# Kernel optimization log

Hardware: AMD Instinct MI355X
Metric: run time of the kernel (lower is better)

The kernel has to match this reference:

```python
import jax, jax.numpy as jnp
import numpy as np
from jax import lax

T, B, I, N, C, L = 512, 256, 64, 512, 10, 3
TAU = 2.0  # train_tau=False -> constant, non-trainable


def setup_inputs() -> dict:
    key = jax.random.key(0)
    ks = jax.random.split(key, 12)
    f32 = jnp.float32
    data = jax.random.normal(ks[0], (T, B, I), f32)
    h0 = 0.1 * jax.random.uniform(ks[1], (L, B, N), f32)  # matches 0.1*torch.rand init
    # Linear params; weights stored as [in, out] so y = x @ W + b
    Win = jax.random.normal(ks[2], (I, N), f32) / np.float32(np.sqrt(I))
    b_in = 0.01 * jax.random.normal(ks[3], (N,), f32)
    Whh = jax.random.normal(ks[4], (L, N, N), f32) / np.float32(np.sqrt(N))
    b_hh = 0.01 * jax.random.normal(ks[5], (L, N), f32)
    Whi = jax.random.normal(ks[6], (L - 1, N, N), f32) / np.float32(np.sqrt(N))
    b_hi = 0.01 * jax.random.normal(ks[7], (L - 1, N), f32)
    Wfc = jax.random.normal(ks[8], (N, C), f32) / np.float32(np.sqrt(N))
    b_fc = 0.01 * jax.random.normal(ks[9], (C,), f32)
    return {"data": data, "h0": h0, "Win": Win, "b_in": b_in,
            "Whh": Whh, "b_hh": b_hh, "Whi": Whi, "b_hi": b_hi,
            "Wfc": Wfc, "b_fc": b_fc}


def reference(data, h0, Win, b_in, Whh, b_hh, Whi, b_hi, Wfc, b_fc):
    alpha = 1.0 - 1.0 / TAU
    # forward() zeroes the recurrent diagonal every call
    Whh = Whh * (1.0 - jnp.eye(N, dtype=Whh.dtype))
    x = data @ Win + b_in  # [T, B, N] input projection (single input layer, mean over 1)

    def step(hs, inp):
        h0_, h1_, h2_ = hs
        # layer 0: leaky integration + LeakyReLU; same inp fed to every layer
        n0 = jax.nn.leaky_relu(alpha * h0_ + (h0_ @ Whh[0] + b_hh[0] + inp) / TAU)
        # layer 1 sees the *updated* layer-0 state (sequential within a timestep)
        n1 = jax.nn.leaky_relu(
            alpha * h1_ + (h1_ @ Whh[1] + b_hh[1] + n0 @ Whi[0] + b_hi[0] + inp) / TAU)
        n2 = jax.nn.leaky_relu(
            alpha * h2_ + (h2_ @ Whh[2] + b_hh[2] + n1 @ Whi[1] + b_hi[1] + inp) / TAU)
        return (n0, n1, n2), None

    hs_final, _ = lax.scan(step, (h0[0], h0[1], h0[2]), x)
    out = hs_final[-1] @ Wfc + b_fc  # [B, C], single readout head
    return out
```

## Files before the change

kernel.cpp:

```cpp
#include <hip/hip_runtime.h>
#include <stdint.h>


#define TS    512
#define BB    256
#define NN    512
#define MR    16
#define NRG   16
#define NCT   4
#define RD    8

#define SW(r, c) (((r) << 9) + ((((c) ^ ((r) & 7))) << 3))

typedef __attribute__((ext_vector_type(8))) short s8v;
typedef __attribute__((ext_vector_type(4))) float f4v;
typedef __attribute__((ext_vector_type(4))) unsigned int u4v;

#define MFMA16(a, b, c) __builtin_amdgcn_mfma_f32_16x16x32_bf16((a), (b), (c), 0, 0, 0)

__device__ __forceinline__ short f2bf(float f) {
  union { float f; unsigned u; } v; v.f = f;
  unsigned u = v.u;
  u += 0x7fffu + ((u >> 16) & 1u);
  return (short)(u >> 16);
}

__device__ __forceinline__ s8v pack8(f4v a, f4v b) {
  s8v v;
  v[0] = f2bf(a[0]); v[1] = f2bf(a[1]); v[2] = f2bf(a[2]); v[3] = f2bf(a[3]);
  v[4] = f2bf(b[0]); v[5] = f2bf(b[1]); v[6] = f2bf(b[2]); v[7] = f2bf(b[3]);
  return v;
}

__device__ __forceinline__ void ld8_sync(u4v o[8],
    unsigned v0, unsigned v1, unsigned v2, unsigned v3,
    const unsigned short* sq, const unsigned short* sp) {
  asm volatile(
      "global_load_dwordx4 %0, %8, %12 sc1\n\t"
      "global_load_dwordx4 %1, %9, %12 sc1\n\t"
      "global_load_dwordx4 %2, %10, %12 sc1\n\t"
      "global_load_dwordx4 %3, %11, %12 sc1\n\t"
      "global_load_dwordx4 %4, %8, %13 sc1\n\t"
      "global_load_dwordx4 %5, %9, %13 sc1\n\t"
      "global_load_dwordx4 %6, %10, %13 sc1\n\t"
      "global_load_dwordx4 %7, %11, %13 sc1\n\t"
      "s_waitcnt vmcnt(0)"
      : "=&v"(o[0]), "=&v"(o[1]), "=&v"(o[2]), "=&v"(o[3]),
        "=&v"(o[4]), "=&v"(o[5]), "=&v"(o[6]), "=&v"(o[7])
      : "v"(v0), "v"(v1), "v"(v2), "v"(v3), "s"(sq), "s"(sp)
      : "memory");
}
__device__ __forceinline__ void ld4_sync(u4v o[4],
    unsigned v0, unsigned v1, unsigned v2, unsigned v3,
    const unsigned short* sb) {
  asm volatile(
      "global_load_dwordx4 %0, %4, %8 sc1\n\t"
      "global_load_dwordx4 %1, %5, %8 sc1\n\t"
      "global_load_dwordx4 %2, %6, %8 sc1\n\t"
      "global_load_dwordx4 %3, %7, %8 sc1\n\t"
      "s_waitcnt vmcnt(0)"
      : "=&v"(o[0]), "=&v"(o[1]), "=&v"(o[2]), "=&v"(o[3])
      : "v"(v0), "v"(v1), "v"(v2), "v"(v3), "s"(sb)
      : "memory");
}

__device__ __forceinline__ void stg_sc1_b16(unsigned short* p, unsigned v) {
  asm volatile("global_store_short %0, %1, off sc1" :: "v"(p), "v"(v) : "memory");
}
__device__ __forceinline__ void waitvm0() {
  asm volatile("s_waitcnt vmcnt(0)" ::: "memory");
}

__global__ __launch_bounds__(256, 1) void rnn_pipe(
    const float* __restrict__ data, const float* __restrict__ h0,
    const float* __restrict__ Win,  const float* __restrict__ b_in,
    const float* __restrict__ Whh,  const float* __restrict__ b_hh,
    const float* __restrict__ Whi,  const float* __restrict__ b_hi,
    unsigned short* __restrict__ ring, unsigned* __restrict__ cnt,
    float* __restrict__ hfinal)
{
  __shared__ __attribute__((aligned(16))) unsigned short qtile[MR * NN];
  __shared__ __attribute__((aligned(16))) unsigned short ptile[MR * NN];

  const int bi   = blockIdx.x;
  const int lay  = bi % 3;
  const int rest = bi / 3;
  const int rg   = rest & 15;
  const int ct   = rest >> 4;
  const int tid  = threadIdx.x;
  const int wv   = tid >> 6;
  const int lane = tid & 63;
  const int lo   = lane & 15;
  const int q4   = lane >> 4;
  const int row0 = rg * MR;
  const int cw   = ct * 128 + wv * 32;

  const int sidx = (lay * NRG + rg) * NCT + ct;
  unsigned* selfprod = cnt + (size_t)sidx * 32;
  unsigned* selfdone = cnt + (size_t)(256 + sidx) * 32;

  unsigned* pollptr = selfprod;
  int polltype = 0;
  if (lane < 4) {
    pollptr = cnt + (size_t)((lay * NRG + rg) * NCT + lane) * 32;  polltype = 1;
  } else if (lane >= 4 && lane < 8 && lay > 0) {
    pollptr = cnt + (size_t)(((lay - 1) * NRG + rg) * NCT + (lane - 4)) * 32;  polltype = 2;
  } else if (lane >= 8 && lane < 12 && lay < 2) {
    pollptr = cnt + (size_t)(256 + ((lay + 1) * NRG + rg) * NCT + (lane - 8)) * 32;  polltype = 3;
  }

  s8v WH[16][2];
  s8v WI[16][2];
  s8v WX[2][2];
  float biasv[2];
  f4v  hst[2];

  {
    const float* WmH = Whh + (size_t)lay * NN * NN;
    #pragma unroll
    for (int kk = 0; kk < 16; ++kk) {
      #pragma unroll
      for (int nf = 0; nf < 2; ++nf) {
        const int col = cw + nf * 16 + lo;
        s8v v;
        #pragma unroll
        for (int j = 0; j < 8; ++j) {
          const int k = kk * 32 + q4 * 8 + j;
          float f = WmH[(size_t)k * NN + col];
          if (k == col) f = 0.f;
          v[j] = f2bf(f);
        }
        WH[kk][nf] = v;
      }
    }
    if (lay > 0) {
      const float* WmI = Whi + (size_t)(lay - 1) * NN * NN;
      #pragma unroll
      for (int kk = 0; kk < 16; ++kk) {
        #pragma unroll
        for (int nf = 0; nf < 2; ++nf) {
          const int col = cw + nf * 16 + lo;
          s8v v;
          #pragma unroll
          for (int j = 0; j < 8; ++j)
            v[j] = f2bf(WmI[(size_t)(kk * 32 + q4 * 8 + j) * NN + col]);
          WI[kk][nf] = v;
        }
      }
    }
    #pragma unroll
    for (int kk = 0; kk < 2; ++kk) {
      #pragma unroll
      for (int nf = 0; nf < 2; ++nf) {
        const int col = cw + nf * 16 + lo;
        s8v v;
        #pragma unroll
        for (int j = 0; j < 8; ++j)
          v[j] = f2bf(Win[(size_t)(kk * 32 + q4 * 8 + j) * NN + col]);
        WX[kk][nf] = v;
      }
    }
    #pragma unroll
    for (int nf = 0; nf < 2; ++nf) {
      const int col = cw + nf * 16 + lo;
      float b = b_hh[lay * NN + col] + b_in[col];
      if (lay > 0) b += b_hi[(lay - 1) * NN + col];
      biasv[nf] = b;
      #pragma unroll
      for (int r = 0; r < 4; ++r)
        hst[nf][r] = h0[(size_t)lay * BB * NN + (size_t)(row0 + q4 * 4 + r) * NN + col];
    }
  }

  const size_t myring = (size_t)(lay * NRG + rg) * RD;
  const size_t upring = (size_t)((lay - 1) * NRG + rg) * RD;

  unsigned voff0 = (unsigned)((0 * 256 + tid) * 16);
  unsigned voff1 = (unsigned)((1 * 256 + tid) * 16);
  unsigned voff2 = (unsigned)((2 * 256 + tid) * 16);
  unsigned voff3 = (unsigned)((3 * 256 + tid) * 16);

  f4v xa0, xa1, xa2, xa3;
  {
    const float* dsrc = data + ((size_t)0 * BB + row0 + lo) * 64 + q4 * 8;
    xa0 = *(const f4v*)(dsrc + 0);
    xa1 = *(const f4v*)(dsrc + 4);
    xa2 = *(const f4v*)(dsrc + 32);
    xa3 = *(const f4v*)(dsrc + 36);
  }

  for (int t = 0; t < TS; ++t) {
    f4v zero4 = {0.f, 0.f, 0.f, 0.f};
    f4v accQ[2] = {zero4, zero4};
    f4v accP[2] = {zero4, zero4};
    {
      s8v xv0 = pack8(xa0, xa1);
      s8v xv1 = pack8(xa2, xa3);
      accQ[0] = MFMA16(xv0, WX[0][0], accQ[0]);
      accQ[1] = MFMA16(xv0, WX[0][1], accQ[1]);
      accQ[0] = MFMA16(xv1, WX[1][0], accQ[0]);
      accQ[1] = MFMA16(xv1, WX[1][1], accQ[1]);
    }

    unsigned tgt = 0;
    if (polltype == 1) tgt = (unsigned)t;
    else if (polltype == 2) tgt = (unsigned)(t + 1);
    else if (polltype == 3 && t >= RD) tgt = (unsigned)(t - RD + 1);
    for (;;) {
      unsigned v = __hip_atomic_load(pollptr, __ATOMIC_RELAXED, __HIP_MEMORY_SCOPE_AGENT);
      if (__all((int)(v >= tgt))) break;
    }

    {
      const unsigned short* qsrc = ring + (myring + ((t - 1) & (RD - 1))) * (MR * NN);
      const unsigned short* psrc = ring + (upring + (t & (RD - 1))) * (MR * NN);
      u4v st[8];
      if (t >= 1 && lay > 0) {
        ld8_sync(st, voff0, voff1, voff2, voff3, qsrc, psrc);
        #pragma unroll
        for (int i = 0; i < 4; ++i) {
          const int g = i * 256 + tid;
          const int r = g >> 6, c = g & 63;
          *(u4v*)(qtile + SW(r, c)) = st[i];
          *(u4v*)(ptile + SW(r, c)) = st[4 + i];
        }
      } else if (t >= 1) {
        ld4_sync(st, voff0, voff1, voff2, voff3, qsrc);
        #pragma unroll
        for (int i = 0; i < 4; ++i) {
          const int g = i * 256 + tid;
          const int r = g >> 6, c = g & 63;
          *(u4v*)(qtile + SW(r, c)) = st[i];
        }
      } else if (lay > 0) {
        ld4_sync(st, voff0, voff1, voff2, voff3, psrc);
        #pragma unroll
        for (int i = 0; i < 4; ++i) {
          const int g = i * 256 + tid;
          const int r = g >> 6, c = g & 63;
          *(u4v*)(ptile + SW(r, c)) = st[i];
        }
      }
    }
    __syncthreads();
    if (tid == 0 && lay > 0)
      __hip_atomic_store(selfdone, (unsigned)(t + 1), __ATOMIC_RELAXED,
                         __HIP_MEMORY_SCOPE_AGENT);

    if (lay > 0) {
      #pragma unroll
      for (int kk = 0; kk < 16; ++kk) {
        s8v av = *(const s8v*)(ptile + SW(lo, kk * 4 + q4));
        accP[0] = MFMA16(av, WI[kk][0], accP[0]);
        accP[1] = MFMA16(av, WI[kk][1], accP[1]);
      }
    }
    if (t == 0) {
      const float* hsrc = h0 + (size_t)lay * BB * NN + (size_t)(row0 + lo) * NN + q4 * 8;
      #pragma unroll
      for (int kk = 0; kk < 16; ++kk) {
        f4v a = *(const f4v*)(hsrc + kk * 32);
        f4v b = *(const f4v*)(hsrc + kk * 32 + 4);
        s8v av = pack8(a, b);
        accQ[0] = MFMA16(av, WH[kk][0], accQ[0]);
        accQ[1] = MFMA16(av, WH[kk][1], accQ[1]);
      }
    } else {
      #pragma unroll
      for (int kk = 0; kk < 16; ++kk) {
        s8v av = *(const s8v*)(qtile + SW(lo, kk * 4 + q4));
        accQ[0] = MFMA16(av, WH[kk][0], accQ[0]);
        accQ[1] = MFMA16(av, WH[kk][1], accQ[1]);
      }
    }

    {
      unsigned short* rslot = ring + (myring + (t & (RD - 1))) * (MR * NN);
      #pragma unroll
      for (int nf = 0; nf < 2; ++nf) {
        const int col = cw + nf * 16 + lo;
        #pragma unroll
        for (int r = 0; r < 4; ++r) {
          const int row = q4 * 4 + r;
          float v = 0.5f * hst[nf][r] + 0.5f * (accQ[nf][r] + accP[nf][r] + biasv[nf]);
          v = (v >= 0.f) ? v : 0.01f * v;
          hst[nf][r] = v;
          stg_sc1_b16(rslot + (size_t)row * NN + col,
                      (unsigned)(unsigned short)f2bf(v));
          if (lay == 2 && t == TS - 1)
            hfinal[(size_t)(row0 + row) * NN + col] = v;
        }
      }
    }

    {
      const int tn = (t + 1 < TS) ? t + 1 : t;
      const float* dsrc = data + ((size_t)tn * BB + row0 + lo) * 64 + q4 * 8;
      xa0 = *(const f4v*)(dsrc + 0);
      xa1 = *(const f4v*)(dsrc + 4);
      xa2 = *(const f4v*)(dsrc + 32);
      xa3 = *(const f4v*)(dsrc + 36);
    }
    waitvm0();
    __syncthreads();
    if (tid == 0)
      __hip_atomic_store(selfprod, (unsigned)(t + 1), __ATOMIC_RELAXED,
                         __HIP_MEMORY_SCOPE_AGENT);
  }
}

__global__ void readout_k(const float* __restrict__ hfinal, const float* __restrict__ Wfc,
                          const float* __restrict__ b_fc, float* __restrict__ out)
{
  const int row = blockIdx.x;
  const int lane = threadIdx.x;
  float a[10];
  #pragma unroll
  for (int c = 0; c < 10; ++c) a[c] = 0.f;
  for (int k = lane; k < NN; k += 64) {
    const float h = hfinal[(size_t)row * NN + k];
    const float* w = Wfc + (size_t)k * 10;
    #pragma unroll
    for (int c = 0; c < 10; ++c) a[c] += h * w[c];
  }
  #pragma unroll
  for (int off = 32; off > 0; off >>= 1) {
    #pragma unroll
    for (int c = 0; c < 10; ++c) a[c] += __shfl_down(a[c], off);
  }
  if (lane == 0) {
    #pragma unroll
    for (int c = 0; c < 10; ++c) out[row * 10 + c] = a[c] + b_fc[c];
  }
}

extern "C" void kernel_launch(void* const* d_in, const int* in_sizes, int n_in,
                              void* d_out, int out_size, void* d_ws, size_t ws_size,
                              hipStream_t stream) {
  (void)in_sizes; (void)n_in; (void)out_size; (void)ws_size;
  const float* data = (const float*)d_in[0];
  const float* h0   = (const float*)d_in[1];
  const float* Win  = (const float*)d_in[2];
  const float* b_in = (const float*)d_in[3];
  const float* Whh  = (const float*)d_in[4];
  const float* b_hh = (const float*)d_in[5];
  const float* Whi  = (const float*)d_in[6];
  const float* b_hi = (const float*)d_in[7];
  const float* Wfc  = (const float*)d_in[8];
  const float* b_fc = (const float*)d_in[9];

  unsigned short* ring = (unsigned short*)d_ws;
  const size_t ring_bytes = (size_t)3 * NRG * RD * MR * NN * 2;
  unsigned* cnt = (unsigned*)((char*)d_ws + ring_bytes);
  float* hfinal = (float*)((char*)d_ws + ring_bytes + 65536);

  hipMemsetAsync(cnt, 0, 65536, stream);
  hipLaunchKernelGGL(rnn_pipe, dim3(192), dim3(256), 0, stream,
                     data, h0, Win, b_in, Whh, b_hh, Whi, b_hi, ring, cnt, hfinal);
  hipLaunchKernelGGL(readout_k, dim3(256), dim3(64), 0, stream,
                     hfinal, Wfc, b_fc, (float*)d_out);
}
```

Baseline: 2.207 ms.

## Co-locate row-group blocks on one XCD and use L2-only coherence when verified

Block indices are remapped so that the 12 blocks sharing a row group are meant to land on the same XCD, assuming round-robin dispatch by blockIdx mod 8. At startup the kernel reads the hardware XCC ID and runs a store/load ring handshake to check that all peers share an XCD and that sc0 loads see neighbour writes. If both checks pass, it uses a template path where flag polling, ring loads and stores skip the sc1 system-coherence bits and use plain stores plus sc0 loads, which cuts cross-die coherence cost on every timestep. It adds a startup handshake and an extra memset, and its correctness depends on the runtime placement check.

```diff
diff --git a/kernel.cpp b/kernel.cpp
--- a/kernel.cpp
+++ b/kernel.cpp
@@ -32,62 +32,106 @@
   return v;
 }
 
-__device__ __forceinline__ void ld8_sync(u4v o[8],
+__device__ __forceinline__ void waitvm0() {
+  asm volatile("s_waitcnt vmcnt(0)" ::: "memory");
+}
+
+__device__ __forceinline__ unsigned ld_sc0_u32(const unsigned* p) {
+  unsigned v;
+  asm volatile("global_load_dword %0, %1, off sc0\n\ts_waitcnt vmcnt(0)"
+               : "=v"(v) : "v"(p) : "memory");
+  return v;
+}
+__device__ __forceinline__ void st_plain_u32(unsigned* p, unsigned v) {
+  asm volatile("global_store_dword %0, %1, off" :: "v"(p), "v"(v) : "memory");
+}
+__device__ __forceinline__ void st_plain_b16(unsigned short* p, unsigned v) {
+  asm volatile("global_store_short %0, %1, off" :: "v"(p), "v"(v) : "memory");
+}
+__device__ __forceinline__ void stg_sc1_b16(unsigned short* p, unsigned v) {
+  asm volatile("global_store_short %0, %1, off sc1" :: "v"(p), "v"(v) : "memory");
+}
+__device__ __forceinline__ unsigned agent_ld(const unsigned* p) {
+  return __hip_atomic_load(p, __ATOMIC_RELAXED, __HIP_MEMORY_SCOPE_AGENT);
+}
+__device__ __forceinline__ void agent_st(unsigned* p, unsigned v) {
+  __hip_atomic_store(p, v, __ATOMIC_RELAXED, __HIP_MEMORY_SCOPE_AGENT);
+}
+
+template<bool FAST>
+__device__ __forceinline__ void ld8p(u4v o[8],
     unsigned v0, unsigned v1, unsigned v2, unsigned v3,
     const unsigned short* sq, const unsigned short* sp) {
-  asm volatile(
-      "global_load_dwordx4 %0, %8, %12 sc1\n\t"
-      "global_load_dwordx4 %1, %9, %12 sc1\n\t"
-      "global_load_dwordx4 %2, %10, %12 sc1\n\t"
-      "global_load_dwordx4 %3, %11, %12 sc1\n\t"
-      "global_load_dwordx4 %4, %8, %13 sc1\n\t"
-      "global_load_dwordx4 %5, %9, %13 sc1\n\t"
-      "global_load_dwordx4 %6, %10, %13 sc1\n\t"
-      "global_load_dwordx4 %7, %11, %13 sc1\n\t"
-      "s_waitcnt vmcnt(0)"
-      : "=&v"(o[0]), "=&v"(o[1]), "=&v"(o[2]), "=&v"(o[3]),
-        "=&v"(o[4]), "=&v"(o[5]), "=&v"(o[6]), "=&v"(o[7])
-      : "v"(v0), "v"(v1), "v"(v2), "v"(v3), "s"(sq), "s"(sp)
-      : "memory");
-}
-__device__ __forceinline__ void ld4_sync(u4v o[4],
+  if constexpr (FAST) {
+    asm volatile(
+        "global_load_dwordx4 %0, %8, %12 sc0\n\t"
+        "global_load_dwordx4 %1, %9, %12 sc0\n\t"
+        "global_load_dwordx4 %2, %10, %12 sc0\n\t"
+        "global_load_dwordx4 %3, %11, %12 sc0\n\t"
+        "global_load_dwordx4 %4, %8, %13 sc0\n\t"
+        "global_load_dwordx4 %5, %9, %13 sc0\n\t"
+        "global_load_dwordx4 %6, %10, %13 sc0\n\t"
+        "global_load_dwordx4 %7, %11, %13 sc0\n\t"
+        "s_waitcnt vmcnt(0)"
+        : "=&v"(o[0]), "=&v"(o[1]), "=&v"(o[2]), "=&v"(o[3]),
+          "=&v"(o[4]), "=&v"(o[5]), "=&v"(o[6]), "=&v"(o[7])
+        : "v"(v0), "v"(v1), "v"(v2), "v"(v3), "s"(sq), "s"(sp)
+        : "memory");
+  } else {
+    asm volatile(
+        "global_load_dwordx4 %0, %8, %12 sc1\n\t"
+        "global_load_dwordx4 %1, %9, %12 sc1\n\t"
+        "global_load_dwordx4 %2, %10, %12 sc1\n\t"
+        "global_load_dwordx4 %3, %11, %12 sc1\n\t"
+        "global_load_dwordx4 %4, %8, %13 sc1\n\t"
+        "global_load_dwordx4 %5, %9, %13 sc1\n\t"
+        "global_load_dwordx4 %6, %10, %13 sc1\n\t"
+        "global_load_dwordx4 %7, %11, %13 sc1\n\t"
+        "s_waitcnt vmcnt(0)"
+        : "=&v"(o[0]), "=&v"(o[1]), "=&v"(o[2]), "=&v"(o[3]),
+          "=&v"(o[4]), "=&v"(o[5]), "=&v"(o[6]), "=&v"(o[7])
+        : "v"(v0), "v"(v1), "v"(v2), "v"(v3), "s"(sq), "s"(sp)
+        : "memory");
+  }
+}
+template<bool FAST>
+__device__ __forceinline__ void ld4p(u4v o[4],
     unsigned v0, unsigned v1, unsigned v2, unsigned v3,
     const unsigned short* sb) {
-  asm volatile(
-      "global_load_dwordx4 %0, %4, %8 sc1\n\t"
-      "global_load_dwordx4 %1, %5, %8 sc1\n\t"
-      "global_load_dwordx4 %2, %6, %8 sc1\n\t"
-      "global_load_dwordx4 %3, %7, %8 sc1\n\t"
-      "s_waitcnt vmcnt(0)"
-      : "=&v"(o[0]), "=&v"(o[1]), "=&v"(o[2]), "=&v"(o[3])
-      : "v"(v0), "v"(v1), "v"(v2), "v"(v3), "s"(sb)
-      : "memory");
-}
-
-__device__ __forceinline__ void stg_sc1_b16(unsigned short* p, unsigned v) {
-  asm volatile("global_store_short %0, %1, off sc1" :: "v"(p), "v"(v) : "memory");
-}
-__device__ __forceinline__ void waitvm0() {
-  asm volatile("s_waitcnt vmcnt(0)" ::: "memory");
-}
-
-__global__ __launch_bounds__(256, 1) void rnn_pipe(
+  if constexpr (FAST) {
+    asm volatile(
+        "global_load_dwordx4 %0, %4, %8 sc0\n\t"
+        "global_load_dwordx4 %1, %5, %8 sc0\n\t"
+        "global_load_dwordx4 %2, %6, %8 sc0\n\t"
+        "global_load_dwordx4 %3, %7, %8 sc0\n\t"
+        "s_waitcnt vmcnt(0)"
+        : "=&v"(o[0]), "=&v"(o[1]), "=&v"(o[2]), "=&v"(o[3])
+        : "v"(v0), "v"(v1), "v"(v2), "v"(v3), "s"(sb)
+        : "memory");
+  } else {
+    asm volatile(
+        "global_load_dwordx4 %0, %4, %8 sc1\n\t"
+        "global_load_dwordx4 %1, %5, %8 sc1\n\t"
+        "global_load_dwordx4 %2, %6, %8 sc1\n\t"
+        "global_load_dwordx4 %3, %7, %8 sc1\n\t"
+        "s_waitcnt vmcnt(0)"
+        : "=&v"(o[0]), "=&v"(o[1]), "=&v"(o[2]), "=&v"(o[3])
+        : "v"(v0), "v"(v1), "v"(v2), "v"(v3), "s"(sb)
+        : "memory");
+  }
+}
+
+template<bool FAST>
+__device__ __forceinline__ void run_all(
     const float* __restrict__ data, const float* __restrict__ h0,
     const float* __restrict__ Win,  const float* __restrict__ b_in,
     const float* __restrict__ Whh,  const float* __restrict__ b_hh,
     const float* __restrict__ Whi,  const float* __restrict__ b_hi,
     unsigned short* __restrict__ ring, unsigned* __restrict__ cnt,
-    float* __restrict__ hfinal)
+    float* __restrict__ hfinal,
+    int lay, int rg, int ct, int tid,
+    unsigned short* qtile, unsigned short* ptile)
 {
-  __shared__ __attribute__((aligned(16))) unsigned short qtile[MR * NN];
-  __shared__ __attribute__((aligned(16))) unsigned short ptile[MR * NN];
-
-  const int bi   = blockIdx.x;
-  const int lay  = bi % 3;
-  const int rest = bi / 3;
-  const int rg   = rest & 15;
-  const int ct   = rest >> 4;
-  const int tid  = threadIdx.x;
   const int wv   = tid >> 6;
   const int lane = tid & 63;
   const int lo   = lane & 15;
@@ -207,7 +251,9 @@
     else if (polltype == 2) tgt = (unsigned)(t + 1);
     else if (polltype == 3 && t >= RD) tgt = (unsigned)(t - RD + 1);
     for (;;) {
-      unsigned v = __hip_atomic_load(pollptr, __ATOMIC_RELAXED, __HIP_MEMORY_SCOPE_AGENT);
+      unsigned v;
+      if constexpr (FAST) v = ld_sc0_u32(pollptr);
+      else                v = agent_ld(pollptr);
       if (__all((int)(v >= tgt))) break;
     }
 
@@ -216,7 +262,7 @@
       const unsigned short* psrc = ring + (upring + (t & (RD - 1))) * (MR * NN);
       u4v st[8];
       if (t >= 1 && lay > 0) {
-        ld8_sync(st, voff0, voff1, voff2, voff3, qsrc, psrc);
+        ld8p<FAST>(st, voff0, voff1, voff2, voff3, qsrc, psrc);
         #pragma unroll
         for (int i = 0; i < 4; ++i) {
           const int g = i * 256 + tid;
@@ -225,7 +271,7 @@
           *(u4v*)(ptile + SW(r, c)) = st[4 + i];
         }
       } else if (t >= 1) {
-        ld4_sync(st, voff0, voff1, voff2, voff3, qsrc);
+        ld4p<FAST>(st, voff0, voff1, voff2, voff3, qsrc);
         #pragma unroll
         for (int i = 0; i < 4; ++i) {
           const int g = i * 256 + tid;
@@ -233,7 +279,7 @@
           *(u4v*)(qtile + SW(r, c)) = st[i];
         }
       } else if (lay > 0) {
-        ld4_sync(st, voff0, voff1, voff2, voff3, psrc);
+        ld4p<FAST>(st, voff0, voff1, voff2, voff3, psrc);
         #pragma unroll
         for (int i = 0; i < 4; ++i) {
           const int g = i * 256 + tid;
@@ -243,9 +289,10 @@
       }
     }
     __syncthreads();
-    if (tid == 0 && lay > 0)
-      __hip_atomic_store(selfdone, (unsigned)(t + 1), __ATOMIC_RELAXED,
-                         __HIP_MEMORY_SCOPE_AGENT);
+    if (tid == 0 && lay > 0) {
+      if constexpr (FAST) st_plain_u32(selfdone, (unsigned)(t + 1));
+      else                agent_st(selfdone, (unsigned)(t + 1));
+    }
 
     if (lay > 0) {
       #pragma unroll
@@ -285,8 +332,12 @@
           float v = 0.5f * hst[nf][r] + 0.5f * (accQ[nf][r] + accP[nf][r] + biasv[nf]);
           v = (v >= 0.f) ? v : 0.01f * v;
           hst[nf][r] = v;
-          stg_sc1_b16(rslot + (size_t)row * NN + col,
-                      (unsigned)(unsigned short)f2bf(v));
+          if constexpr (FAST)
+            st_plain_b16(rslot + (size_t)row * NN + col,
+                         (unsigned)(unsigned short)f2bf(v));
+          else
+            stg_sc1_b16(rslot + (size_t)row * NN + col,
+                        (unsigned)(unsigned short)f2bf(v));
           if (lay == 2 && t == TS - 1)
             hfinal[(size_t)(row0 + row) * NN + col] = v;
         }
@@ -303,10 +354,91 @@
     }
     waitvm0();
     __syncthreads();
-    if (tid == 0)
-      __hip_atomic_store(selfprod, (unsigned)(t + 1), __ATOMIC_RELAXED,
-                         __HIP_MEMORY_SCOPE_AGENT);
-  }
+    if (tid == 0) {
+      if constexpr (FAST) st_plain_u32(selfprod, (unsigned)(t + 1));
+      else                agent_st(selfprod, (unsigned)(t + 1));
+    }
+  }
+}
+
+__global__ __launch_bounds__(256, 1) void rnn_pipe(
+    const float* __restrict__ data, const float* __restrict__ h0,
+    const float* __restrict__ Win,  const float* __restrict__ b_in,
+    const float* __restrict__ Whh,  const float* __restrict__ b_hh,
+    const float* __restrict__ Whi,  const float* __restrict__ b_hi,
+    unsigned short* __restrict__ ring, unsigned* __restrict__ cnt,
+    float* __restrict__ hfinal, unsigned* __restrict__ comm)
+{
+  __shared__ __attribute__((aligned(16))) unsigned short qtile[MR * NN];
+  __shared__ __attribute__((aligned(16))) unsigned short ptile[MR * NN];
+
+  const int bi = blockIdx.x;
+  const int x8   = bi & 7;
+  const int rr   = bi >> 3;
+  const int half = (rr >= 12) ? 1 : 0;
+  const int m    = rr - half * 12;
+  const int rg   = x8 * 2 + half;
+  const int lay  = m >> 2;
+  const int ct   = m & 3;
+  const int tid  = threadIdx.x;
+  const int wv   = tid >> 6;
+  const int lane = tid & 63;
+
+  unsigned* XID = comm;
+  unsigned* TST = comm + 192 * 32;
+  unsigned* PH  = comm + 384 * 32;
+  unsigned* OKA = comm + 576 * 32;
+  const int me  = rg * 12 + m;
+  const int nbi = rg * 12 + ((m + 1) % 12);
+  const int pvi = rg * 12 + ((m + 11) % 12);
+
+  unsigned myx;
+  asm volatile("s_getreg_b32 %0, hwreg(HW_REG_XCC_ID)" : "=s"(myx));
+
+  if (wv == 0) {
+    if (lane == 0) agent_st(XID + (size_t)me * 32, 0x100u | myx);
+    unsigned v = 0x100u | myx;
+    for (;;) {
+      if (lane < 12) v = agent_ld(XID + (size_t)(rg * 12 + lane) * 32);
+      if (__all((int)(v >= 0x100u))) break;
+    }
+    const int same = __all((int)((lane < 12) ? (v == (0x100u | myx)) : 1));
+
+    unsigned r1, r2, r3;
+    if (lane == 0) { st_plain_u32(TST + (size_t)me * 32, 0xA5A50001u); waitvm0();
+                     agent_st(PH + (size_t)me * 32, 1u); }
+    while (agent_ld(PH + (size_t)nbi * 32) < 1u) {}
+    r1 = ld_sc0_u32(TST + (size_t)nbi * 32);
+    if (lane == 0) agent_st(PH + (size_t)me * 32, 2u);
+    while (agent_ld(PH + (size_t)pvi * 32) < 2u) {}
+    if (lane == 0) { st_plain_u32(TST + (size_t)me * 32, 0x5A5A0002u); waitvm0();
+                     agent_st(PH + (size_t)me * 32, 3u); }
+    while (agent_ld(PH + (size_t)nbi * 32) < 3u) {}
+    r2 = ld_sc0_u32(TST + (size_t)nbi * 32);
+    if (lane == 0) agent_st(PH + (size_t)me * 32, 4u);
+    while (agent_ld(PH + (size_t)pvi * 32) < 4u) {}
+    if (lane == 0) { st_plain_u32(TST + (size_t)me * 32, 0x3C3C0003u); waitvm0();
+                     agent_st(PH + (size_t)me * 32, 5u); }
+    while (agent_ld(PH + (size_t)nbi * 32) < 5u) {}
+    r3 = ld_sc0_u32(TST + (size_t)nbi * 32);
+
+    int ok = same && (r1 == 0xA5A50001u) && (r2 == 0x5A5A0002u) && (r3 == 0x3C3C0003u);
+    ok = __all(ok) ? 1 : 0;
+    if (lane == 0) agent_st(OKA + (size_t)me * 32, 0x10u | (unsigned)ok);
+  }
+  unsigned ov = 0x11u;
+  for (;;) {
+    if (lane < 12) ov = agent_ld(OKA + (size_t)(rg * 12 + lane) * 32);
+    if (__all((int)(ov & 0x10u))) break;
+  }
+  const int fast = __all((int)(ov & 1u));
+
+  if (fast)
+    run_all<true >(data, h0, Win, b_in, Whh, b_hh, Whi, b_hi, ring, cnt, hfinal,
+                   lay, rg, ct, tid, qtile, ptile);
+  else
+    run_all<false>(data, h0, Win, b_in, Whh, b_hh, Whi, b_hi, ring, cnt, hfinal,
+                   lay, rg, ct, tid, qtile, ptile);
 }
 
 __global__ void readout_k(const float* __restrict__ hfinal, const float* __restrict__ Wfc,
@@ -353,10 +485,12 @@
   const size_t ring_bytes = (size_t)3 * NRG * RD * MR * NN * 2;
   unsigned* cnt = (unsigned*)((char*)d_ws + ring_bytes);
   float* hfinal = (float*)((char*)d_ws + ring_bytes + 65536);
+  unsigned* comm = (unsigned*)((char*)d_ws + ring_bytes + 65536 + 512 * 1024);
 
   hipMemsetAsync(cnt, 0, 65536, stream);
+  hipMemsetAsync(comm, 0, 98304, stream);
   hipLaunchKernelGGL(rnn_pipe, dim3(192), dim3(256), 0, stream,
-                     data, h0, Win, b_in, Whh, b_hh, Whi, b_hi, ring, cnt, hfinal);
+                     data, h0, Win, b_in, Whh, b_hh, Whi, b_hi, ring, cnt, hfinal, comm);
   hipLaunchKernelGGL(readout_k, dim3(256), dim3(64), 0, stream,
                      hfinal, Wfc, b_fc, (float*)d_out);
 }
```

Result: faster. 2.082 ms (-5.7%).

## Pack bf16 ring stores into dword writes and remap blocks to co-locate row groups

Applied to the files above, without the earlier changes.

Neighbouring lanes now exchange bf16 values with a shuffle so that one lane of each pair writes a 32-bit word to the ring buffer instead of every lane writing a 16-bit store. This halves the number of sc1 global stores on the per-timestep critical path. The block-index mapping also changes so that the layers and column tiles of the same row group sit at nearby block IDs, which likely places communicating blocks on the same XCD and shares L2 traffic. The other edits only wrap the atomic load and store calls in helpers.

```diff
diff --git a/kernel.cpp b/kernel.cpp
--- a/kernel.cpp
+++ b/kernel.cpp
@@ -30,6 +30,20 @@
   v[0] = f2bf(a[0]); v[1] = f2bf(a[1]); v[2] = f2bf(a[2]); v[3] = f2bf(a[3]);
   v[4] = f2bf(b[0]); v[5] = f2bf(b[1]); v[6] = f2bf(b[2]); v[7] = f2bf(b[3]);
   return v;
+}
+
+__device__ __forceinline__ void waitvm0() {
+  asm volatile("s_waitcnt vmcnt(0)" ::: "memory");
+}
+
+__device__ __forceinline__ void stg_sc1_b32(unsigned short* p, unsigned v) {
+  asm volatile("global_store_dword %0, %1, off sc1" :: "v"(p), "v"(v) : "memory");
+}
+__device__ __forceinline__ unsigned agent_ld(const unsigned* p) {
+  return __hip_atomic_load(p, __ATOMIC_RELAXED, __HIP_MEMORY_SCOPE_AGENT);
+}
+__device__ __forceinline__ void agent_st(unsigned* p, unsigned v) {
+  __hip_atomic_store(p, v, __ATOMIC_RELAXED, __HIP_MEMORY_SCOPE_AGENT);
 }
 
 __device__ __forceinline__ void ld8_sync(u4v o[8],
@@ -64,13 +78,6 @@
       : "memory");
 }
 
-__device__ __forceinline__ void stg_sc1_b16(unsigned short* p, unsigned v) {
-  asm volatile("global_store_short %0, %1, off sc1" :: "v"(p), "v"(v) : "memory");
-}
-__device__ __forceinline__ void waitvm0() {
-  asm volatile("s_waitcnt vmcnt(0)" ::: "memory");
-}
-
 __global__ __launch_bounds__(256, 1) void rnn_pipe(
     const float* __restrict__ data, const float* __restrict__ h0,
     const float* __restrict__ Win,  const float* __restrict__ b_in,
@@ -83,10 +90,13 @@
   __shared__ __attribute__((aligned(16))) unsigned short ptile[MR * NN];
 
   const int bi   = blockIdx.x;
-  const int lay  = bi % 3;
-  const int rest = bi / 3;
-  const int rg   = rest & 15;
-  const int ct   = rest >> 4;
+  const int x8   = bi & 7;
+  const int rr   = bi >> 3;
+  const int half = (rr >= 12) ? 1 : 0;
+  const int m    = rr - half * 12;
+  const int rg   = x8 * 2 + half;
+  const int lay  = m >> 2;
+  const int ct   = m & 3;
   const int tid  = threadIdx.x;
   const int wv   = tid >> 6;
   const int lane = tid & 63;
@@ -207,7 +217,7 @@
     else if (polltype == 2) tgt = (unsigned)(t + 1);
     else if (polltype == 3 && t >= RD) tgt = (unsigned)(t - RD + 1);
     for (;;) {
-      unsigned v = __hip_atomic_load(pollptr, __ATOMIC_RELAXED, __HIP_MEMORY_SCOPE_AGENT);
+      unsigned v = agent_ld(pollptr);
       if (__all((int)(v >= tgt))) break;
     }
 
@@ -244,8 +254,7 @@
     }
     __syncthreads();
     if (tid == 0 && lay > 0)
-      __hip_atomic_store(selfdone, (unsigned)(t + 1), __ATOMIC_RELAXED,
-                         __HIP_MEMORY_SCOPE_AGENT);
+      agent_st(selfdone, (unsigned)(t + 1));
 
     if (lay > 0) {
       #pragma unroll
@@ -276,19 +285,22 @@
 
     {
       unsigned short* rslot = ring + (myring + (t & (RD - 1))) * (MR * NN);
+      const int elo = lo & ~1;
       #pragma unroll
       for (int nf = 0; nf < 2; ++nf) {
-        const int col = cw + nf * 16 + lo;
         #pragma unroll
         for (int r = 0; r < 4; ++r) {
           const int row = q4 * 4 + r;
           float v = 0.5f * hst[nf][r] + 0.5f * (accQ[nf][r] + accP[nf][r] + biasv[nf]);
           v = (v >= 0.f) ? v : 0.01f * v;
           hst[nf][r] = v;
-          stg_sc1_b16(rslot + (size_t)row * NN + col,
-                      (unsigned)(unsigned short)f2bf(v));
           if (lay == 2 && t == TS - 1)
-            hfinal[(size_t)(row0 + row) * NN + col] = v;
+            hfinal[(size_t)(row0 + row) * NN + (cw + nf * 16 + lo)] = v;
+          unsigned b  = (unsigned)(unsigned short)f2bf(v);
+          unsigned ob = (unsigned)__shfl_xor((int)b, 1);
+          unsigned word = (lo & 1) ? (ob | (b << 16)) : (b | (ob << 16));
+          if ((lo & 1) == nf)
+            stg_sc1_b32(rslot + (size_t)row * NN + (cw + nf * 16 + elo), word);
         }
       }
     }
@@ -304,8 +316,7 @@
     waitvm0();
     __syncthreads();
     if (tid == 0)
-      __hip_atomic_store(selfprod, (unsigned)(t + 1), __ATOMIC_RELAXED,
-                         __HIP_MEMORY_SCOPE_AGENT);
+      agent_st(selfprod, (unsigned)(t + 1));
   }
 }
 
```

Measured after the change: 2.270 ms. 1.03x slower.
